# Kernel optimization log

Measured on AMD Instinct MI355X. Metric: run time of the kernel, lower is better.

Reference implementation:

```python
import jax, jax.numpy as jnp
import numpy as np

NEG_SLOPE = 0.2  # PyG GATConv default negative_slope


def gat_conv(x, W, b, a_src, a_dst, src, dst, N, H, C):
    """PyG-style GATConv (v1 attention), concat heads, self-loops already in (src,dst)."""
    h = (x @ W).reshape(N, H, C)                       # [N,H,C]
    al_src = jnp.sum(h * a_src, axis=-1)               # [N,H]
    al_dst = jnp.sum(h * a_dst, axis=-1)               # [N,H]
    e = jax.nn.leaky_relu(al_src[src] + al_dst[dst], NEG_SLOPE)  # [E,H]
    m = jax.ops.segment_max(e, dst, num_segments=N)    # segment softmax (stable)
    m = jnp.where(jnp.isfinite(m), m, 0.0)
    ex = jnp.exp(e - m[dst])
    denom = jax.ops.segment_sum(ex, dst, num_segments=N)
    alpha = ex / (denom[dst] + 1e-16)                  # [E,H]
    msg = h[src] * alpha[..., None]                    # [E,H,C]
    out = jax.ops.segment_sum(msg, dst, num_segments=N)  # [N,H,C]
    return out.reshape(N, H * C) + b


def setup_inputs() -> dict:
    key = jax.random.key(0)
    ks = jax.random.split(key, 16)
    N, E, IN, HID, HEADS, OUT, G = 50000, 600000, 128, 64, 4, 10, 64
    x = jax.random.normal(ks[0], (N, IN), dtype=jnp.float32)
    edge_index = jax.random.randint(ks[1], (2, E), 0, N, dtype=jnp.int32)
    batch = jnp.sort(jax.random.randint(ks[2], (N,), 0, G, dtype=jnp.int32))
    s = 0.1
    p = {
        'W1': jax.random.normal(ks[3], (IN, HEADS * HID)) * s,
        'b1': jnp.zeros((HEADS * HID,), jnp.float32),
        'asrc1': jax.random.normal(ks[4], (HEADS, HID)) * s,
        'adst1': jax.random.normal(ks[5], (HEADS, HID)) * s,
        'W2': jax.random.normal(ks[6], (HEADS * HID, HEADS * HID)) * s,
        'b2': jnp.zeros((HEADS * HID,), jnp.float32),
        'asrc2': jax.random.normal(ks[7], (HEADS, HID)) * s,
        'adst2': jax.random.normal(ks[8], (HEADS, HID)) * s,
        'W3': jax.random.normal(ks[9], (HEADS * HID, HID)) * s,
        'b3': jnp.zeros((HID,), jnp.float32),
        'asrc3': jax.random.normal(ks[10], (1, HID)) * s,
        'adst3': jax.random.normal(ks[11], (1, HID)) * s,
        'linW': jax.random.normal(ks[12], (HID, OUT)) * s,
        'linb': jnp.zeros((OUT,), jnp.float32),
    }
    return dict(x=x, edge_index=edge_index, batch=batch, **p)


def reference(x, edge_index, batch, W1, b1, asrc1, adst1, W2, b2, asrc2, adst2,
              W3, b3, asrc3, adst3, linW, linb):
    N = x.shape[0]
    G = 64  # number of graphs
    loops = jnp.arange(N, dtype=edge_index.dtype)
    src = jnp.concatenate([edge_index[0], loops])  # PyG adds self-loops by default
    dst = jnp.concatenate([edge_index[1], loops])
    # eval mode: dropout is identity
    h = jax.nn.elu(gat_conv(x, W1, b1, asrc1, adst1, src, dst, N, 4, 64))
    h = jax.nn.elu(gat_conv(h, W2, b2, asrc2, adst2, src, dst, N, 4, 64))
    h = jax.nn.elu(gat_conv(h, W3, b3, asrc3, adst3, src, dst, N, 1, 64))
    # global mean pool over graphs
    sums = jax.ops.segment_sum(h, batch, num_segments=G)            # [G,64]
    cnts = jax.ops.segment_sum(jnp.ones((N,), h.dtype), batch, num_segments=G)
    pooled = sums / jnp.maximum(cnts, 1.0)[:, None]
    return pooled @ linW + linb                                      # [G,10]
```

## Files before the change

kernel.cpp:

```cpp
#include <hip/hip_runtime.h>
#include <hip/hip_bf16.h>
#include <math.h>

#define NEG_SLOPE 0.2f

typedef short short8 __attribute__((ext_vector_type(8)));
typedef float f32x4 __attribute__((ext_vector_type(4)));
typedef unsigned int u32;
typedef unsigned short u16;

__device__ __forceinline__ float lrelu(float x){ return x > 0.f ? x : NEG_SLOPE * x; }
__device__ __forceinline__ float elu_f(float x){ return x > 0.f ? x : __expf(x) - 1.f; }
__device__ __forceinline__ float blo(u32 w){ return __uint_as_float(w << 16); }
__device__ __forceinline__ float bhi(u32 w){ return __uint_as_float(w & 0xffff0000u); }
__device__ __forceinline__ float bf2f(u16 u){ return __uint_as_float(((u32)u) << 16); }
__device__ __forceinline__ u16 f2bf(float f){
  __hip_bfloat16 h = __float2bfloat16(f);
  return *(u16*)&h;
}

__global__ void prep_kernel(const float* __restrict__ x, u16* __restrict__ xb, int n4,
                            const float* __restrict__ W1, u16* __restrict__ w1t,
                            const float* __restrict__ W2, u16* __restrict__ w2t,
                            const float* __restrict__ W3, u16* __restrict__ w3t,
                            int* __restrict__ cursor, int N,
                            float* __restrict__ sums, int* __restrict__ cnts){
  int i = blockIdx.x * 256 + threadIdx.x;
  if (i < n4){
    float4 v = ((const float4*)x)[i];
    ushort4 o;
    o.x = f2bf(v.x); o.y = f2bf(v.y); o.z = f2bf(v.z); o.w = f2bf(v.w);
    ((ushort4*)xb)[i] = o;
    return;
  }
  int t = i - n4;
  if (t < 128 * 256){
    int k = t >> 8, m = t & 255;
    w1t[m * 128 + k] = f2bf(W1[t]);
    return;
  }
  t -= 128 * 256;
  if (t < 256 * 256){
    int k = t >> 8, m = t & 255;
    w2t[m * 256 + k] = f2bf(W2[t]);
    return;
  }
  t -= 256 * 256;
  if (t < 256 * 64){
    int k = t >> 6, m = t & 63;
    w3t[m * 256 + k] = f2bf(W3[t]);
    return;
  }
  t -= 256 * 64;
  if (t < N){ cursor[t] = 0; return; }
  t -= N;
  if (t < 64 * 64){ sums[t] = 0.f; return; }
  t -= 64 * 64;
  if (t < 64) cnts[t] = 0;
}

__global__ void ell_kernel(const int* __restrict__ src, const int* __restrict__ dst,
                           int E, int* cursor, int* __restrict__ ell){
  int i = blockIdx.x * 256 + threadIdx.x;
  if (i < E){
    int s = src[i], d = dst[i];
    int pos = atomicAdd(&cursor[d], 1);
    if (pos < 64) ell[(size_t)d * 64 + pos] = s;
  }
}

template<int BM, int BN>
__global__ __launch_bounds__((BN == 256) ? 512 : 256) void gemm_mfma(
    const u16* __restrict__ A, const u16* __restrict__ Bt, u16* __restrict__ C,
    const float* __restrict__ asrc, const float* __restrict__ adst,
    float* __restrict__ als, float* __restrict__ ald, int N, int K, int M){
  constexpr int T   = (BN == 256) ? 512 : 256;
  constexpr int MI  = (BN == 256) ? (BM / 32) : (BM / 64);
  constexpr int HH  = BN / 64;
  constexpr int AQ  = BM * 8 / T;
  constexpr int SB  = BN * 8 / T;
  constexpr int LB  = (BN == 256) ? 8 : 6;
  constexpr int LBM = (BM == 128) ? 7 : 6;
  __shared__ short As[8][BM][8];
  __shared__ short Bs[8][BN][8];
  const int tid = threadIdx.x;
  const int w = tid >> 6, lane = tid & 63;
  const int quad = lane >> 4, l16 = lane & 15;
  const int row0 = blockIdx.y * BM;
  const int wrow = (BN == 256) ? (w >> 2) * (BM / 2) : w * (BM / 4);
  const int wcol = (BN == 256) ? (w & 3) * 64 : 0;

  f32x4 acc[MI][4];
#pragma unroll
  for (int i = 0; i < MI; i++)
#pragma unroll
    for (int j = 0; j < 4; j++) acc[i][j] = (f32x4){0.f, 0.f, 0.f, 0.f};

  for (int k0 = 0; k0 < K; k0 += 64){
    __syncthreads();
#pragma unroll
    for (int q = 0; q < AQ; q++){
      int lb = q * T + w * 64;
      int li = lb + lane;
      int c = li >> LBM, r = li & (BM - 1);
      int grow = min(row0 + r, N - 1);
      const u16* gp = A + (size_t)grow * K + k0 + c * 8;
      __builtin_amdgcn_global_load_lds((const __attribute__((address_space(1))) void*)gp,
                                       (__attribute__((address_space(3))) void*)((char*)&As[0][0][0] + (size_t)lb * 16),
                                       16, 0, 0);
    }
#pragma unroll
    for (int q = 0; q < SB; q++){
      int lb = q * T + w * 64;
      int li = lb + lane;
      int c = li >> LB, n = li & (BN - 1);
      const u16* gp = Bt + (size_t)n * K + k0 + c * 8;
      __builtin_amdgcn_global_load_lds((const __attribute__((address_space(1))) void*)gp,
                                       (__attribute__((address_space(3))) void*)((char*)&Bs[0][0][0] + (size_t)lb * 16),
                                       16, 0, 0);
    }
    __syncthreads();
#pragma unroll
    for (int ks = 0; ks < 2; ks++){
      short8 a[MI], b[4];
#pragma unroll
      for (int i = 0; i < MI; i++) a[i] = *(const short8*)&As[ks * 4 + quad][wrow + i * 16 + l16][0];
#pragma unroll
      for (int j = 0; j < 4; j++)  b[j] = *(const short8*)&Bs[ks * 4 + quad][wcol + j * 16 + l16][0];
#pragma unroll
      for (int i = 0; i < MI; i++)
#pragma unroll
        for (int j = 0; j < 4; j++)
          acc[i][j] = __builtin_amdgcn_mfma_f32_16x16x32_bf16(a[i], b[j], acc[i][j], 0, 0, 0);
    }
  }

  const int head = wcol >> 6;
  float avs[4], avd[4];
#pragma unroll
  for (int j = 0; j < 4; j++){
    int c = j * 16 + l16;
    avs[j] = asrc[head * 64 + c];
    avd[j] = adst[head * 64 + c];
  }

#pragma unroll
  for (int i = 0; i < MI; i++){
#pragma unroll
    for (int rr = 0; rr < 4; rr++){
      int row = row0 + wrow + i * 16 + quad * 4 + rr;
      float ps = acc[i][0][rr] * avs[0] + acc[i][1][rr] * avs[1]
               + acc[i][2][rr] * avs[2] + acc[i][3][rr] * avs[3];
      float pd = acc[i][0][rr] * avd[0] + acc[i][1][rr] * avd[1]
               + acc[i][2][rr] * avd[2] + acc[i][3][rr] * avd[3];
#pragma unroll
      for (int off = 8; off > 0; off >>= 1){
        ps += __shfl_xor(ps, off);
        pd += __shfl_xor(pd, off);
      }
      if (row < N){
#pragma unroll
        for (int j = 0; j < 4; j++)
          C[(size_t)row * M + wcol + j * 16 + l16] = f2bf(acc[i][j][rr]);
        if (l16 == 0){
          als[(size_t)row * HH + head] = ps;
          ald[(size_t)row * HH + head] = pd;
        }
      }
    }
  }
}

__global__ __launch_bounds__(256) void agg4_kernel(const u16* __restrict__ hb,
    const float* __restrict__ als, const float* __restrict__ ald,
    const int* __restrict__ degv, const int* __restrict__ ell,
    const float* __restrict__ bias, u16* __restrict__ out, int N){
  __shared__ float lex[4][256];
  __shared__ int lu[4][64];
  int wslot = threadIdx.x >> 6;
  int node = (blockIdx.x * 256 + threadIdx.x) >> 6;
  int lane = threadIdx.x & 63;
  if (node >= N) return;
  int deg = min(degv[node], 64);
  float4 t4 = *(const float4*)(ald + node * 4);
  const int hh = lane >> 4;

  bool v = lane < deg;
  int u = v ? ell[(size_t)node * 64 + lane] : 0;
  float4 s = *(const float4*)(als + (size_t)u * 4);
  float4 exv;
  exv.x = v ? __expf(lrelu(s.x + t4.x)) : 0.f;
  exv.y = v ? __expf(lrelu(s.y + t4.y)) : 0.f;
  exv.z = v ? __expf(lrelu(s.z + t4.z)) : 0.f;
  exv.w = v ? __expf(lrelu(s.w + t4.w)) : 0.f;
  *(float4*)&lex[wslot][lane * 4] = exv;
  lu[wslot][lane] = u;
  asm volatile("s_waitcnt lgkmcnt(0)" ::: "memory");

  const u16* hbl = hb + lane * 4;
  float4 ss = *(const float4*)(als + (size_t)node * 4);
  float es0 = __expf(lrelu(ss.x + t4.x));
  float es1 = __expf(lrelu(ss.y + t4.y));
  float es2 = __expf(lrelu(ss.z + t4.z));
  float es3 = __expf(lrelu(ss.w + t4.w));
  float exs = (hh == 0) ? es0 : (hh == 1) ? es1 : (hh == 2) ? es2 : es3;
  uint2 tself = *(const uint2*)(hbl + (size_t)node * 256);
  float denom = exs;
  float a0 = exs * blo(tself.x), a1 = exs * bhi(tself.x);
  float a2 = exs * blo(tself.y), a3 = exs * bhi(tself.y);

#pragma unroll 8
  for (int jj = 0; jj < deg; jj++){
    float ex = lex[wslot][jj * 4 + hh];
    int uu = lu[wslot][jj];
    uint2 t = *(const uint2*)(hbl + (size_t)uu * 256);
    denom += ex;
    a0 += ex * blo(t.x);
    a1 += ex * bhi(t.x);
    a2 += ex * blo(t.y);
    a3 += ex * bhi(t.y);
  }
  float inv = 1.f / (denom + 1e-16f);
  int ch = lane * 4;
  float o0 = elu_f(a0 * inv + bias[ch]);
  float o1 = elu_f(a1 * inv + bias[ch + 1]);
  float o2 = elu_f(a2 * inv + bias[ch + 2]);
  float o3 = elu_f(a3 * inv + bias[ch + 3]);
  uint2 o;
  o.x = (u32)f2bf(o0) | ((u32)f2bf(o1) << 16);
  o.y = (u32)f2bf(o2) | ((u32)f2bf(o3) << 16);
  ((uint2*)out)[(size_t)node * 64 + lane] = o;
}

__global__ __launch_bounds__(256) void agg1_kernel(const u16* __restrict__ hb,
    const float* __restrict__ als, const float* __restrict__ ald,
    const int* __restrict__ degv, const int* __restrict__ ell,
    const float* __restrict__ bias, u16* __restrict__ out, int N){
  __shared__ float lex[4][72];
  __shared__ int lu[4][72];
  int wslot = threadIdx.x >> 6;
  int node = (blockIdx.x * 256 + threadIdx.x) >> 6;
  int lane = threadIdx.x & 63;
  if (node >= N) return;
  int deg = min(degv[node], 64);
  float adv = ald[node];

  bool v = lane < deg;
  int u = v ? ell[(size_t)node * 64 + lane] : 0;
  lex[wslot][lane] = v ? __expf(lrelu(als[u] + adv)) : 0.f;
  lu[wslot][lane] = u;
  if (lane < 8){ lex[wslot][64 + lane] = 0.f; lu[wslot][64 + lane] = 0; }
  asm volatile("s_waitcnt lgkmcnt(0)" ::: "memory");

  int eo = lane >> 4;
  int chb = (lane & 15) * 4;
  float a0 = 0.f, a1 = 0.f, a2 = 0.f, a3 = 0.f, denom = 0.f;
  if (eo == 0){
    float exs = __expf(lrelu(als[node] + adv));
    uint2 t = *(const uint2*)(hb + (size_t)node * 64 + chb);
    denom = exs;
    a0 = exs * blo(t.x); a1 = exs * bhi(t.x);
    a2 = exs * blo(t.y); a3 = exs * bhi(t.y);
  }
#pragma unroll 4
  for (int j2 = 0; j2 < deg; j2 += 4){
    int jj = j2 + eo;
    float ex = lex[wslot][jj];
    int uu = lu[wslot][jj];
    uint2 t = *(const uint2*)(hb + (size_t)uu * 64 + chb);
    denom += ex;
    a0 += ex * blo(t.x);
    a1 += ex * bhi(t.x);
    a2 += ex * blo(t.y);
    a3 += ex * bhi(t.y);
  }
#pragma unroll
  for (int off = 16; off < 64; off <<= 1){
    denom += __shfl_xor(denom, off);
    a0 += __shfl_xor(a0, off); a1 += __shfl_xor(a1, off);
    a2 += __shfl_xor(a2, off); a3 += __shfl_xor(a3, off);
  }
  if (eo == 0){
    float inv = 1.f / (denom + 1e-16f);
    float o0 = elu_f(a0 * inv + bias[chb]);
    float o1 = elu_f(a1 * inv + bias[chb + 1]);
    float o2 = elu_f(a2 * inv + bias[chb + 2]);
    float o3 = elu_f(a3 * inv + bias[chb + 3]);
    uint2 o;
    o.x = (u32)f2bf(o0) | ((u32)f2bf(o1) << 16);
    o.y = (u32)f2bf(o2) | ((u32)f2bf(o3) << 16);
    *(uint2*)(out + (size_t)node * 64 + chb) = o;
  }
}

__global__ void pool_kernel(const u16* __restrict__ f, const int* __restrict__ batch,
                            float* sums, int* cnts, int N){
  int lane = threadIdx.x;
  int s = blockIdx.x * 128;
  if (s >= N) return;
  int e = min(s + 128, N);
  float acc = 0.f;
  int cnt = 0;
  int cur = batch[s];
  for (int n = s; n < e; n++){
    int g = batch[n];
    if (g != cur){
      atomicAdd(&sums[cur * 64 + lane], acc);
      if (lane == 0) atomicAdd(&cnts[cur], cnt);
      acc = 0.f; cnt = 0; cur = g;
    }
    acc += bf2f(f[(size_t)n * 64 + lane]);
    cnt++;
  }
  atomicAdd(&sums[cur * 64 + lane], acc);
  if (lane == 0) atomicAdd(&cnts[cur], cnt);
}

__global__ void final_kernel(const float* __restrict__ sums, const int* __restrict__ cnts,
                             const float* __restrict__ linW, const float* __restrict__ linb,
                             float* __restrict__ out){
  int t = threadIdx.x;
  if (t >= 640) return;
  int g = t / 10, o = t % 10;
  float c = fmaxf((float)cnts[g], 1.f);
  float acc = 0.f;
#pragma unroll
  for (int k = 0; k < 64; k++) acc += sums[g * 64 + k] * linW[k * 10 + o];
  out[t] = acc / c + linb[o];
}

extern "C" void kernel_launch(void* const* d_in, const int* in_sizes, int n_in,
                              void* d_out, int out_size, void* d_ws, size_t ws_size,
                              hipStream_t stream) {
  const float* x     = (const float*)d_in[0];
  const int*   ei    = (const int*)  d_in[1];
  const int*   batch = (const int*)  d_in[2];
  const float* W1    = (const float*)d_in[3];
  const float* b1    = (const float*)d_in[4];
  const float* asrc1 = (const float*)d_in[5];
  const float* adst1 = (const float*)d_in[6];
  const float* W2    = (const float*)d_in[7];
  const float* b2    = (const float*)d_in[8];
  const float* asrc2 = (const float*)d_in[9];
  const float* adst2 = (const float*)d_in[10];
  const float* W3    = (const float*)d_in[11];
  const float* b3    = (const float*)d_in[12];
  const float* asrc3 = (const float*)d_in[13];
  const float* adst3 = (const float*)d_in[14];
  const float* linW  = (const float*)d_in[15];
  const float* linb  = (const float*)d_in[16];

  const int N = in_sizes[0] / 128;
  const int E = in_sizes[1] / 2;
  const int G = 64;
  const int* src = ei;
  const int* dst = ei + E;

  char* p = (char*)d_ws;
  auto carve = [&](size_t bytes) -> char* {
    char* r = p;
    p += (bytes + 255) & ~(size_t)255;
    return r;
  };
  u16*   xb       = (u16*)  carve((size_t)N * 128 * 2);
  u16*   w1t      = (u16*)  carve((size_t)256 * 128 * 2);
  u16*   w2t      = (u16*)  carve((size_t)256 * 256 * 2);
  u16*   w3t      = (u16*)  carve((size_t)64 * 256 * 2);
  u16*   hb       = (u16*)  carve((size_t)N * 256 * 2);
  u16*   featb    = (u16*)  carve((size_t)N * 256 * 2);
  u16*   out3     = (u16*)  carve((size_t)N * 64 * 2);
  float* als      = (float*)carve((size_t)N * 4 * 4);
  float* ald      = (float*)carve((size_t)N * 4 * 4);
  int*   cursor   = (int*)  carve((size_t)N * 4);
  int*   ell      = (int*)  carve((size_t)N * 64 * 4);
  float* sums     = (float*)carve((size_t)G * 64 * 4);
  int*   cnts     = (int*)  carve((size_t)G * 4);

  const int n4 = N * 128 / 4;
  const int prep_items = n4 + 128 * 256 + 256 * 256 + 256 * 64 + N + G * 64 + G;

  prep_kernel<<<(prep_items + 255) / 256, 256, 0, stream>>>(x, xb, n4, W1, w1t, W2, w2t, W3, w3t,
                                                            cursor, N, sums, cnts);

  ell_kernel<<<(E + 255) / 256, 256, 0, stream>>>(src, dst, E, cursor, ell);

  const int nby64  = (N + 63) / 64;
  const int nby128 = (N + 127) / 128;
  const int wpn_grid = (N + 3) / 4;

  gemm_mfma<64, 256><<<dim3(1, nby64), 512, 0, stream>>>(xb, w1t, hb, asrc1, adst1, als, ald, N, 128, 256);
  agg4_kernel<<<wpn_grid, 256, 0, stream>>>(hb, als, ald, cursor, ell, b1, featb, N);

  gemm_mfma<64, 256><<<dim3(1, nby64), 512, 0, stream>>>(featb, w2t, hb, asrc2, adst2, als, ald, N, 256, 256);
  agg4_kernel<<<wpn_grid, 256, 0, stream>>>(hb, als, ald, cursor, ell, b2, featb, N);

  gemm_mfma<128, 64><<<dim3(1, nby128), 256, 0, stream>>>(featb, w3t, hb, asrc3, adst3, als, ald, N, 256, 64);
  agg1_kernel<<<wpn_grid, 256, 0, stream>>>(hb, als, ald, cursor, ell, b3, out3, N);

  pool_kernel<<<(N + 127) / 128, 64, 0, stream>>>(out3, batch, sums, cnts, N);
  final_kernel<<<1, 640, 0, stream>>>(sums, cnts, linW, linb, (float*)d_out);
}
```

Before: 378.4 us.

## Fuse final aggregation with mean pooling and retune GEMM tile sizes

```diff
diff --git a/kernel.cpp b/kernel.cpp
--- a/kernel.cpp
+++ b/kernel.cpp
@@ -24,7 +24,7 @@
                             const float* __restrict__ W2, u16* __restrict__ w2t,
                             const float* __restrict__ W3, u16* __restrict__ w3t,
                             int* __restrict__ cursor, int N,
-                            float* __restrict__ sums, int* __restrict__ cnts){
+                            float* __restrict__ sums){
   int i = blockIdx.x * 256 + threadIdx.x;
   if (i < n4){
     float4 v = ((const float4*)x)[i];
@@ -54,9 +54,7 @@
   t -= 256 * 64;
   if (t < N){ cursor[t] = 0; return; }
   t -= N;
-  if (t < 64 * 64){ sums[t] = 0.f; return; }
-  t -= 64 * 64;
-  if (t < 64) cnts[t] = 0;
+  if (t < 64 * 64) sums[t] = 0.f;
 }
 
 __global__ void ell_kernel(const int* __restrict__ src, const int* __restrict__ dst,
@@ -232,10 +230,11 @@
   ((uint2*)out)[(size_t)node * 64 + lane] = o;
 }
 
-__global__ __launch_bounds__(256) void agg1_kernel(const u16* __restrict__ hb,
+__global__ __launch_bounds__(256) void agg1pool_kernel(const u16* __restrict__ hb,
     const float* __restrict__ als, const float* __restrict__ ald,
     const int* __restrict__ degv, const int* __restrict__ ell,
-    const float* __restrict__ bias, u16* __restrict__ out, int N){
+    const float* __restrict__ bias, const int* __restrict__ batch,
+    float* __restrict__ sums, int N){
   __shared__ float lex[4][72];
   __shared__ int lu[4][72];
   int wslot = threadIdx.x >> 6;
@@ -282,47 +281,27 @@
   }
   if (eo == 0){
     float inv = 1.f / (denom + 1e-16f);
-    float o0 = elu_f(a0 * inv + bias[chb]);
-    float o1 = elu_f(a1 * inv + bias[chb + 1]);
-    float o2 = elu_f(a2 * inv + bias[chb + 2]);
-    float o3 = elu_f(a3 * inv + bias[chb + 3]);
-    uint2 o;
-    o.x = (u32)f2bf(o0) | ((u32)f2bf(o1) << 16);
-    o.y = (u32)f2bf(o2) | ((u32)f2bf(o3) << 16);
-    *(uint2*)(out + (size_t)node * 64 + chb) = o;
-  }
-}
-
-__global__ void pool_kernel(const u16* __restrict__ f, const int* __restrict__ batch,
-                            float* sums, int* cnts, int N){
-  int lane = threadIdx.x;
-  int s = blockIdx.x * 128;
-  if (s >= N) return;
-  int e = min(s + 128, N);
-  float acc = 0.f;
-  int cnt = 0;
-  int cur = batch[s];
-  for (int n = s; n < e; n++){
-    int g = batch[n];
-    if (g != cur){
-      atomicAdd(&sums[cur * 64 + lane], acc);
-      if (lane == 0) atomicAdd(&cnts[cur], cnt);
-      acc = 0.f; cnt = 0; cur = g;
-    }
-    acc += bf2f(f[(size_t)n * 64 + lane]);
-    cnt++;
-  }
-  atomicAdd(&sums[cur * 64 + lane], acc);
-  if (lane == 0) atomicAdd(&cnts[cur], cnt);
-}
-
-__global__ void final_kernel(const float* __restrict__ sums, const int* __restrict__ cnts,
-                             const float* __restrict__ linW, const float* __restrict__ linb,
-                             float* __restrict__ out){
+    int g = batch[node];
+    float* sp = sums + (size_t)g * 64 + chb;
+    atomicAdd(sp + 0, elu_f(a0 * inv + bias[chb]));
+    atomicAdd(sp + 1, elu_f(a1 * inv + bias[chb + 1]));
+    atomicAdd(sp + 2, elu_f(a2 * inv + bias[chb + 2]));
+    atomicAdd(sp + 3, elu_f(a3 * inv + bias[chb + 3]));
+  }
+}
+
+__global__ void final_kernel(const float* __restrict__ sums, const int* __restrict__ batch,
+                             int N, const float* __restrict__ linW,
+                             const float* __restrict__ linb, float* __restrict__ out){
   int t = threadIdx.x;
   if (t >= 640) return;
   int g = t / 10, o = t % 10;
-  float c = fmaxf((float)cnts[g], 1.f);
+  int lo = 0, hi = N;
+  while (lo < hi){ int mid = (lo + hi) >> 1; if (batch[mid] < g) lo = mid + 1; else hi = mid; }
+  int s0 = lo;
+  lo = 0; hi = N;
+  while (lo < hi){ int mid = (lo + hi) >> 1; if (batch[mid] < g + 1) lo = mid + 1; else hi = mid; }
+  float c = fmaxf((float)(lo - s0), 1.f);
   float acc = 0.f;
 #pragma unroll
   for (int k = 0; k < 64; k++) acc += sums[g * 64 + k] * linW[k * 10 + o];
@@ -368,35 +347,33 @@
   u16*   w3t      = (u16*)  carve((size_t)64 * 256 * 2);
   u16*   hb       = (u16*)  carve((size_t)N * 256 * 2);
   u16*   featb    = (u16*)  carve((size_t)N * 256 * 2);
-  u16*   out3     = (u16*)  carve((size_t)N * 64 * 2);
   float* als      = (float*)carve((size_t)N * 4 * 4);
   float* ald      = (float*)carve((size_t)N * 4 * 4);
   int*   cursor   = (int*)  carve((size_t)N * 4);
   int*   ell      = (int*)  carve((size_t)N * 64 * 4);
   float* sums     = (float*)carve((size_t)G * 64 * 4);
-  int*   cnts     = (int*)  carve((size_t)G * 4);
 
   const int n4 = N * 128 / 4;
-  const int prep_items = n4 + 128 * 256 + 256 * 256 + 256 * 64 + N + G * 64 + G;
+  const int prep_items = n4 + 128 * 256 + 256 * 256 + 256 * 64 + N + G * 64;
 
   prep_kernel<<<(prep_items + 255) / 256, 256, 0, stream>>>(x, xb, n4, W1, w1t, W2, w2t, W3, w3t,
-                                                            cursor, N, sums, cnts);
+                                                            cursor, N, sums);
 
   ell_kernel<<<(E + 255) / 256, 256, 0, stream>>>(src, dst, E, cursor, ell);
 
+  const int nby128 = (N + 127) / 128;
   const int nby64  = (N + 63) / 64;
-  const int nby128 = (N + 127) / 128;
   const int wpn_grid = (N + 3) / 4;
 
-  gemm_mfma<64, 256><<<dim3(1, nby64), 512, 0, stream>>>(xb, w1t, hb, asrc1, adst1, als, ald, N, 128, 256);
+  gemm_mfma<128, 256><<<dim3(1, nby128), 512, 0, stream>>>(xb, w1t, hb, asrc1, adst1, als, ald, N, 128, 256);
   agg4_kernel<<<wpn_grid, 256, 0, stream>>>(hb, als, ald, cursor, ell, b1, featb, N);
 
-  gemm_mfma<64, 256><<<dim3(1, nby64), 512, 0, stream>>>(featb, w2t, hb, asrc2, adst2, als, ald, N, 256, 256);
+  gemm_mfma<128, 256><<<dim3(1, nby128), 512, 0, stream>>>(featb, w2t, hb, asrc2, adst2, als, ald, N, 256, 256);
   agg4_kernel<<<wpn_grid, 256, 0, stream>>>(hb, als, ald, cursor, ell, b2, featb, N);
 
-  gemm_mfma<128, 64><<<dim3(1, nby128), 256, 0, stream>>>(featb, w3t, hb, asrc3, adst3, als, ald, N, 256, 64);
-  agg1_kernel<<<wpn_grid, 256, 0, stream>>>(hb, als, ald, cursor, ell, b3, out3, N);
-
-  pool_kernel<<<(N + 127) / 128, 64, 0, stream>>>(out3, batch, sums, cnts, N);
-  final_kernel<<<1, 640, 0, stream>>>(sums, cnts, linW, linb, (float*)d_out);
-}
+  gemm_mfma<64, 64><<<dim3(1, nby64), 256, 0, stream>>>(featb, w3t, hb, asrc3, adst3, als, ald, N, 256, 64);
+
+  agg1pool_kernel<<<wpn_grid, 256, 0, stream>>>(hb, als, ald, cursor, ell, b3, batch, sums, N);
+
+  final_kernel<<<1, 640, 0, stream>>>(sums, batch, N, linW, linb, (float*)d_out);
+}
```

Result: slower. 557.0 us (+47.2%).
